# Optimization experiments

Measured on AMD Instinct MI355X. Metric: run time of the kernel, lower is better.

The kernel has to match this reference:

```python
import jax, jax.numpy as jnp
import numpy as np

B, T, C = 32, 2048, 1024  # batch, seq_len (<= block_size), n_embd
HEAD_SIZE = 128


def setup_inputs() -> dict:
    key = jax.random.key(0)
    kx, kk, kq, kv = jax.random.split(key, 4)
    std = 0.02  # CustomLinear init: normal(0, 0.02)
    return {
        "x": jax.random.normal(kx, (B, T, C), dtype=jnp.float32),
        "Wk": jax.random.normal(kk, (HEAD_SIZE, C), dtype=jnp.float32) * std,
        "Wq": jax.random.normal(kq, (HEAD_SIZE, C), dtype=jnp.float32) * std,
        "Wv": jax.random.normal(kv, (HEAD_SIZE, C), dtype=jnp.float32) * std,
    }


def reference(x, Wk, Wq, Wv):
    # x: [B, T, C]; W*: [head_size, C] (torch Linear layout, no bias)
    Bb, Tt, Cc = x.shape
    k = jnp.einsum("btc,hc->bth", x, Wk)
    q = jnp.einsum("btc,hc->bth", x, Wq)
    v = jnp.einsum("btc,hc->bth", x, Wv)
    # NOTE: original scales by C**-0.5 (n_embd), not head_size**-0.5
    wei = jnp.einsum("bth,bsh->bts", q, k) * (Cc ** -0.5)
    causal = jnp.tril(jnp.ones((Tt, Tt), dtype=bool))  # tril[:T,:T]
    wei = jnp.where(causal, wei, -jnp.inf)
    wei = jax.nn.softmax(wei, axis=-1)
    return jnp.einsum("bts,bsh->bth", wei, v)  # [B, T, head_size]
```

## Files before the change

kernel.cpp:

```cpp
#include <hip/hip_runtime.h>
#include <hip/hip_bf16.h>

typedef __bf16 bf8_t __attribute__((ext_vector_type(8)));
typedef __bf16 bf4_t __attribute__((ext_vector_type(4)));
typedef float f4_t __attribute__((ext_vector_type(4)));

#define B_ 32
#define T_ 2048
#define C_ 1024
#define H_ 128

__global__ __launch_bounds__(256) void wconv_kernel(
    const float* __restrict__ Wk, const float* __restrict__ Wq, const float* __restrict__ Wv,
    __bf16* __restrict__ Wb)
{
    const int e = (blockIdx.x * 256 + threadIdx.x) * 8;
    const int arr = e >> 17;
    const int off = e & 131071;
    const float* W = (arr == 0) ? Wk : (arr == 1) ? Wq : Wv;
    float4 f0 = *(const float4*)(W + off);
    float4 f1 = *(const float4*)(W + off + 4);
    bf8_t o;
    o[0] = (__bf16)f0.x; o[1] = (__bf16)f0.y; o[2] = (__bf16)f0.z; o[3] = (__bf16)f0.w;
    o[4] = (__bf16)f1.x; o[5] = (__bf16)f1.y; o[6] = (__bf16)f1.z; o[7] = (__bf16)f1.w;
    *(bf8_t*)(Wb + e) = o;
}

__global__ __launch_bounds__(256, 3) void proj_kernel(
    const float* __restrict__ x, const __bf16* __restrict__ Wb,
    __bf16* __restrict__ Kb, __bf16* __restrict__ Qb, __bf16* __restrict__ VtG)
{
    __shared__ __bf16 Xs[64][40];
    __shared__ __bf16 Ws[384][40];

    const int m0   = blockIdx.x * 64;
    const int tid  = threadIdx.x;
    const int lane = tid & 63;
    const int wn   = tid >> 6;
    const int lr   = lane & 15;
    const int quad = lane >> 4;

    f4_t acc[4][6];
    #pragma unroll
    for (int mi = 0; mi < 4; mi++)
        for (int ni = 0; ni < 6; ni++) acc[mi][ni] = f4_t{0.f, 0.f, 0.f, 0.f};

    float4 xr[2];
    bf8_t  wr[6];
    #pragma unroll
    for (int i = 0; i < 2; i++) {
        const int u = tid + i * 256;
        xr[i] = *(const float4*)(x + (size_t)(m0 + (u >> 3)) * C_ + ((u & 7) << 2));
    }
    #pragma unroll
    for (int i = 0; i < 6; i++) {
        const int u = tid + i * 256;
        wr[i] = *(const bf8_t*)(Wb + (size_t)(u >> 2) * C_ + ((u & 3) << 3));
    }

    for (int kkI = 0; kkI < 32; kkI++) {
        __syncthreads();
        #pragma unroll
        for (int i = 0; i < 2; i++) {
            const int u = tid + i * 256;
            float4 f = xr[i];
            *(bf4_t*)&Xs[u >> 3][(u & 7) << 2] =
                bf4_t{(__bf16)f.x, (__bf16)f.y, (__bf16)f.z, (__bf16)f.w};
        }
        #pragma unroll
        for (int i = 0; i < 6; i++) {
            const int u = tid + i * 256;
            *(bf8_t*)&Ws[u >> 2][(u & 3) << 3] = wr[i];
        }
        __syncthreads();
        if (kkI < 31) {
            const int kk = (kkI + 1) * 32;
            #pragma unroll
            for (int i = 0; i < 2; i++) {
                const int u = tid + i * 256;
                xr[i] = *(const float4*)(x + (size_t)(m0 + (u >> 3)) * C_ + kk + ((u & 7) << 2));
            }
            #pragma unroll
            for (int i = 0; i < 6; i++) {
                const int u = tid + i * 256;
                wr[i] = *(const bf8_t*)(Wb + (size_t)(u >> 2) * C_ + kk + ((u & 3) << 3));
            }
        }
        bf8_t xa[4];
        #pragma unroll
        for (int mi = 0; mi < 4; mi++) xa[mi] = *(const bf8_t*)&Xs[mi * 16 + lr][quad * 8];
        #pragma unroll
        for (int ni = 0; ni < 6; ni++) {
            bf8_t wb = *(const bf8_t*)&Ws[ni * 64 + wn * 16 + lr][quad * 8];
            if (ni < 4) {
                #pragma unroll
                for (int mi = 0; mi < 4; mi++)
                    acc[mi][ni] = __builtin_amdgcn_mfma_f32_16x16x32_bf16(xa[mi], wb, acc[mi][ni], 0, 0, 0);
            } else {
                #pragma unroll
                for (int mi = 0; mi < 4; mi++)
                    acc[mi][ni] = __builtin_amdgcn_mfma_f32_16x16x32_bf16(wb, xa[mi], acc[mi][ni], 0, 0, 0);
            }
        }
    }

    const int bb = m0 >> 11;
    const int t0 = m0 & (T_ - 1);
    #pragma unroll
    for (int ni = 0; ni < 4; ni++) {
        __bf16* Out = (ni < 2) ? Kb : Qb;
        const int col = (ni & 1) * 64 + wn * 16 + lr;
        #pragma unroll
        for (int mi = 0; mi < 4; mi++)
            for (int r = 0; r < 4; r++) {
                const int row = m0 + mi * 16 + quad * 4 + r;
                Out[(size_t)row * H_ + col] = (__bf16)acc[mi][ni][r];
            }
    }
    #pragma unroll
    for (int ni = 4; ni < 6; ni++)
        for (int mi = 0; mi < 4; mi++) {
            const int tok = t0 + mi * 16 + lr;
            #pragma unroll
            for (int r = 0; r < 4; r++) {
                const int h = (ni - 4) * 64 + wn * 16 + quad * 4 + r;
                VtG[(size_t)bb * H_ * T_ + (size_t)h * T_ + tok] = (__bf16)acc[mi][ni][r];
            }
        }
}

__global__ __launch_bounds__(512, 4) void flash_kernel(
    const __bf16* __restrict__ Qb, const __bf16* __restrict__ Kb,
    const __bf16* __restrict__ VtG, float* __restrict__ Out)
{
    __shared__ __bf16 Ks[64][136];
    __shared__ __bf16 Vt[128][72];
    __shared__ __bf16 Ps[128][72];

    const int qt = (blockIdx.y < 16) ? (15 - blockIdx.x) : blockIdx.x;
    const int b  = blockIdx.y;
    const size_t kqbase = (size_t)b * T_ * H_;
    const size_t vbase  = (size_t)b * H_ * T_;

    const int tid  = threadIdx.x;
    const int lane = tid & 63;
    const int w    = tid >> 6;
    const int lr   = lane & 15;
    const int quad = lane >> 4;

    bf8_t qf[4];
    {
        const __bf16* qp = Qb + kqbase + (size_t)(qt * 128 + w * 16 + lr) * H_ + quad * 8;
        #pragma unroll
        for (int ks = 0; ks < 4; ks++) qf[ks] = *(const bf8_t*)(qp + ks * 32);
    }

    f4_t o[8];
    #pragma unroll
    for (int n = 0; n < 8; n++) o[n] = f4_t{0.f, 0.f, 0.f, 0.f};
    float ls[4] = {0.f, 0.f, 0.f, 0.f};

    const float sc = 0.03125f * 1.4426950408889634f;
    const int jmax = 2 * qt + 1;

    const int kRow0 = tid >> 4,          kC0 = (tid & 15) << 3;
    const int kRow1 = (tid + 512) >> 4,  kC1 = ((tid + 512) & 15) << 3;
    const int vH0 = tid >> 3,            vS0 = (tid & 7) << 3;
    const int vH1 = (tid + 512) >> 3,    vS1 = ((tid + 512) & 7) << 3;

    bf8_t kr0 = *(const bf8_t*)(Kb + kqbase + (size_t)kRow0 * H_ + kC0);
    bf8_t kr1 = *(const bf8_t*)(Kb + kqbase + (size_t)kRow1 * H_ + kC1);
    bf8_t vr0 = *(const bf8_t*)(VtG + vbase + (size_t)vH0 * T_ + vS0);
    bf8_t vr1 = *(const bf8_t*)(VtG + vbase + (size_t)vH1 * T_ + vS1);

    for (int j = 0; j <= jmax; j++) {
        __syncthreads();
        *(bf8_t*)&Ks[kRow0][kC0] = kr0;
        *(bf8_t*)&Ks[kRow1][kC1] = kr1;
        *(bf8_t*)&Vt[vH0][vS0]   = vr0;
        *(bf8_t*)&Vt[vH1][vS1]   = vr1;
        __syncthreads();
        if (j < jmax) {
            const int s0 = (j + 1) * 64;
            kr0 = *(const bf8_t*)(Kb + kqbase + (size_t)(s0 + kRow0) * H_ + kC0);
            kr1 = *(const bf8_t*)(Kb + kqbase + (size_t)(s0 + kRow1) * H_ + kC1);
            vr0 = *(const bf8_t*)(VtG + vbase + (size_t)vH0 * T_ + s0 + vS0);
            vr1 = *(const bf8_t*)(VtG + vbase + (size_t)vH1 * T_ + s0 + vS1);
        }
        if (j == jmax && w < 4) continue;

        f4_t s4[4];
        #pragma unroll
        for (int n = 0; n < 4; n++) s4[n] = f4_t{0.f, 0.f, 0.f, 0.f};
        #pragma unroll
        for (int ks = 0; ks < 4; ks++)
            for (int n = 0; n < 4; n++) {
                bf8_t kf = *(const bf8_t*)&Ks[n * 16 + lr][ks * 32 + quad * 8];
                s4[n] = __builtin_amdgcn_mfma_f32_16x16x32_bf16(qf[ks], kf, s4[n], 0, 0, 0);
            }

        const bool domask = (j - 2 * qt) == (w >> 2);
        const int rowg = qt * 128 + w * 16 + quad * 4;
        #pragma unroll
        for (int n = 0; n < 4; n++) {
            const int colg = j * 64 + n * 16 + lr;
            #pragma unroll
            for (int r = 0; r < 4; r++) {
                float p = __builtin_exp2f(s4[n][r] * sc);
                if (domask && colg > rowg + r) p = 0.f;
                ls[r] += p;
                Ps[w * 16 + quad * 4 + r][n * 16 + lr] = (__bf16)p;
            }
        }

        #pragma unroll
        for (int ks = 0; ks < 2; ks++) {
            bf8_t pf = *(const bf8_t*)&Ps[w * 16 + lr][ks * 32 + quad * 8];
            #pragma unroll
            for (int n = 0; n < 8; n++) {
                bf8_t vf = *(const bf8_t*)&Vt[n * 16 + lr][ks * 32 + quad * 8];
                o[n] = __builtin_amdgcn_mfma_f32_16x16x32_bf16(pf, vf, o[n], 0, 0, 0);
            }
        }
    }

    float inv[4];
    #pragma unroll
    for (int r = 0; r < 4; r++) {
        float v = ls[r];
        v += __shfl_xor(v, 1);
        v += __shfl_xor(v, 2);
        v += __shfl_xor(v, 4);
        v += __shfl_xor(v, 8);
        inv[r] = 1.f / v;
    }
    #pragma unroll
    for (int n = 0; n < 8; n++) {
        const int col = n * 16 + lr;
        #pragma unroll
        for (int r = 0; r < 4; r++) {
            const int row = qt * 128 + w * 16 + quad * 4 + r;
            Out[kqbase + (size_t)row * H_ + col] = o[n][r] * inv[r];
        }
    }
}

extern "C" void kernel_launch(void* const* d_in, const int* in_sizes, int n_in,
                              void* d_out, int out_size, void* d_ws, size_t ws_size,
                              hipStream_t stream) {
    const float* x  = (const float*)d_in[0];
    const float* Wk = (const float*)d_in[1];
    const float* Wq = (const float*)d_in[2];
    const float* Wv = (const float*)d_in[3];
    float* out = (float*)d_out;

    const size_t n_kqv = (size_t)B_ * T_ * H_;
    __bf16* Kb  = (__bf16*)d_ws;
    __bf16* Qb  = Kb + n_kqv;
    __bf16* VtG = Qb + n_kqv;
    __bf16* Wb  = VtG + n_kqv;

    wconv_kernel<<<dim3(192), 256, 0, stream>>>(Wk, Wq, Wv, Wb);
    proj_kernel<<<dim3((B_ * T_) / 64), 256, 0, stream>>>(x, Wb, Kb, Qb, VtG);
    flash_kernel<<<dim3(16, B_), 512, 0, stream>>>(Qb, Kb, VtG, out);
}
```

Before: 510.2 us.

## Use direct global-to-LDS async loads in fragment-ordered layout for projection and flash

Replaces the register-staged software prefetch in both the projection and flash-attention kernels with global_load_lds direct-to-LDS transfers. Shared memory is reorganised into MFMA fragment order, so each lane reads its operand contiguously and the padded row layouts go away. The projection kernel now stages x in fp32 in LDS and converts it to bf16 at read time. The register double-buffering prefetch is dropped, so loads are no longer overlapped with compute within a block, and each iteration pays a load-then-barrier stall.

Measured after the change: 551.7 us. 1.08x slower.

```diff
diff --git a/kernel.cpp b/kernel.cpp
--- a/kernel.cpp
+++ b/kernel.cpp
@@ -2,13 +2,18 @@
 #include <hip/hip_bf16.h>
 
 typedef __bf16 bf8_t __attribute__((ext_vector_type(8)));
-typedef __bf16 bf4_t __attribute__((ext_vector_type(4)));
 typedef float f4_t __attribute__((ext_vector_type(4)));
 
 #define B_ 32
 #define T_ 2048
 #define C_ 1024
 #define H_ 128
+
+__device__ __forceinline__ void async16(const void* g, void* l) {
+    __builtin_amdgcn_global_load_lds(
+        (const __attribute__((address_space(1))) void*)g,
+        (__attribute__((address_space(3))) void*)l, 16, 0, 0);
+}
 
 __global__ __launch_bounds__(256) void wconv_kernel(
     const float* __restrict__ Wk, const float* __restrict__ Wq, const float* __restrict__ Wv,
@@ -30,8 +35,8 @@
     const float* __restrict__ x, const __bf16* __restrict__ Wb,
     __bf16* __restrict__ Kb, __bf16* __restrict__ Qb, __bf16* __restrict__ VtG)
 {
-    __shared__ __bf16 Xs[64][40];
-    __shared__ __bf16 Ws[384][40];
+    __shared__ __align__(16) float  Xf[4][2][64][4];
+    __shared__ __align__(16) __bf16 Wf[6][4][64][8];
 
     const int m0   = blockIdx.x * 64;
     const int tid  = threadIdx.x;
@@ -45,53 +50,30 @@
     for (int mi = 0; mi < 4; mi++)
         for (int ni = 0; ni < 6; ni++) acc[mi][ni] = f4_t{0.f, 0.f, 0.f, 0.f};
 
-    float4 xr[2];
-    bf8_t  wr[6];
-    #pragma unroll
-    for (int i = 0; i < 2; i++) {
-        const int u = tid + i * 256;
-        xr[i] = *(const float4*)(x + (size_t)(m0 + (u >> 3)) * C_ + ((u & 7) << 2));
-    }
-    #pragma unroll
-    for (int i = 0; i < 6; i++) {
-        const int u = tid + i * 256;
-        wr[i] = *(const bf8_t*)(Wb + (size_t)(u >> 2) * C_ + ((u & 3) << 3));
-    }
-
-    for (int kkI = 0; kkI < 32; kkI++) {
-        __syncthreads();
-        #pragma unroll
-        for (int i = 0; i < 2; i++) {
-            const int u = tid + i * 256;
-            float4 f = xr[i];
-            *(bf4_t*)&Xs[u >> 3][(u & 7) << 2] =
-                bf4_t{(__bf16)f.x, (__bf16)f.y, (__bf16)f.z, (__bf16)f.w};
-        }
-        #pragma unroll
-        for (int i = 0; i < 6; i++) {
-            const int u = tid + i * 256;
-            *(bf8_t*)&Ws[u >> 2][(u & 3) << 3] = wr[i];
-        }
-        __syncthreads();
-        if (kkI < 31) {
-            const int kk = (kkI + 1) * 32;
-            #pragma unroll
-            for (int i = 0; i < 2; i++) {
-                const int u = tid + i * 256;
-                xr[i] = *(const float4*)(x + (size_t)(m0 + (u >> 3)) * C_ + kk + ((u & 7) << 2));
-            }
-            #pragma unroll
-            for (int i = 0; i < 6; i++) {
-                const int u = tid + i * 256;
-                wr[i] = *(const bf8_t*)(Wb + (size_t)(u >> 2) * C_ + kk + ((u & 3) << 3));
-            }
-        }
+    for (int kk = 0; kk < C_; kk += 32) {
+        #pragma unroll
+        for (int c = 0; c < 2; c++)
+            async16(x + (size_t)(m0 + wn * 16 + lr) * C_ + kk + quad * 8 + c * 4,
+                    &Xf[wn][c][lane][0]);
+        #pragma unroll
+        for (int ni = 0; ni < 6; ni++)
+            async16(Wb + (size_t)(ni * 64 + wn * 16 + lr) * C_ + kk + quad * 8,
+                    &Wf[ni][wn][lane][0]);
+        __syncthreads();
+
         bf8_t xa[4];
         #pragma unroll
-        for (int mi = 0; mi < 4; mi++) xa[mi] = *(const bf8_t*)&Xs[mi * 16 + lr][quad * 8];
+        for (int mi = 0; mi < 4; mi++) {
+            float4 a0 = *(const float4*)&Xf[mi][0][lane][0];
+            float4 a1 = *(const float4*)&Xf[mi][1][lane][0];
+            bf8_t t;
+            t[0] = (__bf16)a0.x; t[1] = (__bf16)a0.y; t[2] = (__bf16)a0.z; t[3] = (__bf16)a0.w;
+            t[4] = (__bf16)a1.x; t[5] = (__bf16)a1.y; t[6] = (__bf16)a1.z; t[7] = (__bf16)a1.w;
+            xa[mi] = t;
+        }
         #pragma unroll
         for (int ni = 0; ni < 6; ni++) {
-            bf8_t wb = *(const bf8_t*)&Ws[ni * 64 + wn * 16 + lr][quad * 8];
+            bf8_t wb = *(const bf8_t*)&Wf[ni][wn][lane][0];
             if (ni < 4) {
                 #pragma unroll
                 for (int mi = 0; mi < 4; mi++)
@@ -102,6 +84,7 @@
                     acc[mi][ni] = __builtin_amdgcn_mfma_f32_16x16x32_bf16(wb, xa[mi], acc[mi][ni], 0, 0, 0);
             }
         }
+        __syncthreads();
     }
 
     const int bb = m0 >> 11;
@@ -133,8 +116,8 @@
     const __bf16* __restrict__ Qb, const __bf16* __restrict__ Kb,
     const __bf16* __restrict__ VtG, float* __restrict__ Out)
 {
-    __shared__ __bf16 Ks[64][136];
-    __shared__ __bf16 Vt[128][72];
+    __shared__ __align__(16) __bf16 Kf[4][4][64][8];
+    __shared__ __align__(16) __bf16 Vf[8][2][64][8];
     __shared__ __bf16 Ps[128][72];
 
     const int qt = (blockIdx.y < 16) ? (15 - blockIdx.x) : blockIdx.x;
@@ -163,65 +146,60 @@
     const float sc = 0.03125f * 1.4426950408889634f;
     const int jmax = 2 * qt + 1;
 
-    const int kRow0 = tid >> 4,          kC0 = (tid & 15) << 3;
-    const int kRow1 = (tid + 512) >> 4,  kC1 = ((tid + 512) & 15) << 3;
-    const int vH0 = tid >> 3,            vS0 = (tid & 7) << 3;
-    const int vH1 = (tid + 512) >> 3,    vS1 = ((tid + 512) & 7) << 3;
-
-    bf8_t kr0 = *(const bf8_t*)(Kb + kqbase + (size_t)kRow0 * H_ + kC0);
-    bf8_t kr1 = *(const bf8_t*)(Kb + kqbase + (size_t)kRow1 * H_ + kC1);
-    bf8_t vr0 = *(const bf8_t*)(VtG + vbase + (size_t)vH0 * T_ + vS0);
-    bf8_t vr1 = *(const bf8_t*)(VtG + vbase + (size_t)vH1 * T_ + vS1);
-
     for (int j = 0; j <= jmax; j++) {
-        __syncthreads();
-        *(bf8_t*)&Ks[kRow0][kC0] = kr0;
-        *(bf8_t*)&Ks[kRow1][kC1] = kr1;
-        *(bf8_t*)&Vt[vH0][vS0]   = vr0;
-        *(bf8_t*)&Vt[vH1][vS1]   = vr1;
-        __syncthreads();
-        if (j < jmax) {
-            const int s0 = (j + 1) * 64;
-            kr0 = *(const bf8_t*)(Kb + kqbase + (size_t)(s0 + kRow0) * H_ + kC0);
-            kr1 = *(const bf8_t*)(Kb + kqbase + (size_t)(s0 + kRow1) * H_ + kC1);
-            vr0 = *(const bf8_t*)(VtG + vbase + (size_t)vH0 * T_ + s0 + vS0);
-            vr1 = *(const bf8_t*)(VtG + vbase + (size_t)vH1 * T_ + s0 + vS1);
-        }
-        if (j == jmax && w < 4) continue;
-
-        f4_t s4[4];
-        #pragma unroll
-        for (int n = 0; n < 4; n++) s4[n] = f4_t{0.f, 0.f, 0.f, 0.f};
-        #pragma unroll
-        for (int ks = 0; ks < 4; ks++)
+        const int s0 = j * 64;
+        #pragma unroll
+        for (int i = 0; i < 4; i++) {
+            const int f = w * 4 + i;
+            if (f < 16) {
+                const int n = f >> 2, ks = f & 3;
+                async16(Kb + kqbase + (size_t)(s0 + n * 16 + lr) * H_ + ks * 32 + quad * 8,
+                        &Kf[n][ks][lane][0]);
+            } else {
+                const int g = f - 16, n = g >> 1, ks = g & 1;
+                async16(VtG + vbase + (size_t)(n * 16 + lr) * T_ + s0 + ks * 32 + quad * 8,
+                        &Vf[n][ks][lane][0]);
+            }
+        }
+        __syncthreads();
+
+        const bool skip = (j == jmax && w < 4);
+        if (!skip) {
+            f4_t s4[4];
+            #pragma unroll
+            for (int n = 0; n < 4; n++) s4[n] = f4_t{0.f, 0.f, 0.f, 0.f};
+            #pragma unroll
+            for (int ks = 0; ks < 4; ks++)
+                for (int n = 0; n < 4; n++) {
+                    bf8_t kf = *(const bf8_t*)&Kf[n][ks][lane][0];
+                    s4[n] = __builtin_amdgcn_mfma_f32_16x16x32_bf16(qf[ks], kf, s4[n], 0, 0, 0);
+                }
+
+            const bool domask = (j - 2 * qt) == (w >> 2);
+            const int rowg = qt * 128 + w * 16 + quad * 4;
+            #pragma unroll
             for (int n = 0; n < 4; n++) {
-                bf8_t kf = *(const bf8_t*)&Ks[n * 16 + lr][ks * 32 + quad * 8];
-                s4[n] = __builtin_amdgcn_mfma_f32_16x16x32_bf16(qf[ks], kf, s4[n], 0, 0, 0);
-            }
-
-        const bool domask = (j - 2 * qt) == (w >> 2);
-        const int rowg = qt * 128 + w * 16 + quad * 4;
-        #pragma unroll
-        for (int n = 0; n < 4; n++) {
-            const int colg = j * 64 + n * 16 + lr;
-            #pragma unroll
-            for (int r = 0; r < 4; r++) {
-                float p = __builtin_exp2f(s4[n][r] * sc);
-                if (domask && colg > rowg + r) p = 0.f;
-                ls[r] += p;
-                Ps[w * 16 + quad * 4 + r][n * 16 + lr] = (__bf16)p;
-            }
-        }
-
-        #pragma unroll
-        for (int ks = 0; ks < 2; ks++) {
-            bf8_t pf = *(const bf8_t*)&Ps[w * 16 + lr][ks * 32 + quad * 8];
-            #pragma unroll
-            for (int n = 0; n < 8; n++) {
-                bf8_t vf = *(const bf8_t*)&Vt[n * 16 + lr][ks * 32 + quad * 8];
-                o[n] = __builtin_amdgcn_mfma_f32_16x16x32_bf16(pf, vf, o[n], 0, 0, 0);
-            }
-        }
+                const int colg = s0 + n * 16 + lr;
+                #pragma unroll
+                for (int r = 0; r < 4; r++) {
+                    float p = __builtin_exp2f(s4[n][r] * sc);
+                    if (domask && colg > rowg + r) p = 0.f;
+                    ls[r] += p;
+                    Ps[w * 16 + quad * 4 + r][n * 16 + lr] = (__bf16)p;
+                }
+            }
+
+            #pragma unroll
+            for (int ks = 0; ks < 2; ks++) {
+                bf8_t pf = *(const bf8_t*)&Ps[w * 16 + lr][ks * 32 + quad * 8];
+                #pragma unroll
+                for (int n = 0; n < 8; n++) {
+                    bf8_t vf = *(const bf8_t*)&Vf[n][ks][lane][0];
+                    o[n] = __builtin_amdgcn_mfma_f32_16x16x32_bf16(pf, vf, o[n], 0, 0, 0);
+                }
+            }
+        }
+        __syncthreads();
     }
 
     float inv[4];
```
